# Kernel tuning notes

Measured on AMD Instinct MI355X. Metric: run time of the kernel, lower is better.

The kernel has to match this reference:

```python
import jax, jax.numpy as jnp
import numpy as np

DIM = 768
HEADS = 12
HIDDEN = 3072  # dim * mlp_ratio
EPS = 1e-5


def layernorm(x, g, b):
    mu = jnp.mean(x, axis=-1, keepdims=True)
    var = jnp.var(x, axis=-1, keepdims=True)
    return (x - mu) * jax.lax.rsqrt(var + EPS) * g + b


def setup_inputs() -> dict:
    key = jax.random.key(0)
    ks = jax.random.split(key, 10)
    s = 0.02
    return {
        "x": jax.random.normal(ks[0], (4, 1024, DIM), jnp.float32),
        "attention_mask": jax.random.randint(ks[1], (4, 1024), 0, 2, jnp.int32),
        "ln1_g": jnp.ones((DIM,), jnp.float32),
        "ln1_b": jnp.zeros((DIM,), jnp.float32),
        "ln2_g": jnp.ones((DIM,), jnp.float32),
        "ln2_b": jnp.zeros((DIM,), jnp.float32),
        "w_qkv": jax.random.normal(ks[2], (DIM, 3 * DIM), jnp.float32) * s,
        "b_qkv": jnp.zeros((3 * DIM,), jnp.float32),
        "w_proj": jax.random.normal(ks[3], (DIM, DIM), jnp.float32) * s,
        "b_proj": jnp.zeros((DIM,), jnp.float32),
        "w_fc1": jax.random.normal(ks[4], (DIM, HIDDEN), jnp.float32) * s,
        "b_fc1": jnp.zeros((HIDDEN,), jnp.float32),
        "w_fc2": jax.random.normal(ks[5], (HIDDEN, DIM), jnp.float32) * s,
        "b_fc2": jnp.zeros((DIM,), jnp.float32),
    }


def reference(x, attention_mask, ln1_g, ln1_b, ln2_g, ln2_b,
              w_qkv, b_qkv, w_proj, b_proj, w_fc1, b_fc1, w_fc2, b_fc2):
    B, N, C = x.shape
    hd = C // HEADS
    scale = hd ** -0.5

    # --- attention branch ---
    h = layernorm(x, ln1_g, ln1_b)
    qkv = (h @ w_qkv + b_qkv).reshape(B, N, 3, HEADS, hd)
    q, k, v = qkv[:, :, 0], qkv[:, :, 1], qkv[:, :, 2]  # [B,N,H,hd]
    attn = jnp.einsum('bnhd,bmhd->bhnm', q, k) * scale
    mask_bias = jnp.where(attention_mask == 0, -10000.0, 0.0)[:, None, None, :]
    attn = jax.nn.softmax(attn + mask_bias, axis=-1)
    o = jnp.einsum('bhnm,bmhd->bnhd', attn, v).reshape(B, N, C)
    x = x + (o @ w_proj + b_proj)

    # --- MLP branch ---
    h = layernorm(x, ln2_g, ln2_b)
    h = jax.nn.gelu(h @ w_fc1 + b_fc1, approximate=False)
    x = x + (h @ w_fc2 + b_fc2)
    return x
```

## Files before the change

### kernel.cpp

```cpp
#include <hip/hip_runtime.h>

#define DIM 768
#define NTOK 4096
#define HID 3072

typedef __attribute__((ext_vector_type(8))) short bf16x8;
typedef __attribute__((ext_vector_type(4))) float f32x4;

__device__ inline unsigned short f2bf(float f){
  unsigned u = __float_as_uint(f);
  u += 0x7fff + ((u >> 16) & 1);
  return (unsigned short)(u >> 16);
}
__device__ inline unsigned cvt_pk_bf16(float a, float b){
  unsigned r;
  asm("v_cvt_pk_bf16_f32 %0, %1, %2" : "=v"(r) : "v"(a), "v"(b));
  return r;
}
__device__ inline void gload_lds16(const void* g, void* l){
  __builtin_amdgcn_global_load_lds(
      (const __attribute__((address_space(1))) unsigned int*)g,
      (__attribute__((address_space(3))) unsigned int*)l, 16, 0, 0);
}
template<int N> __device__ inline void wait_vmcnt(){
  if constexpr (N == 0) asm volatile("s_waitcnt vmcnt(0)" ::: "memory");
  else if constexpr (N == 4) asm volatile("s_waitcnt vmcnt(4)" ::: "memory");
  else if constexpr (N == 8) asm volatile("s_waitcnt vmcnt(8)" ::: "memory");
  else static_assert(N == 0, "unsupported vmcnt");
}
__device__ inline int swz_read(int row, int hi){
  return (row * 64 + hi * 16) ^ ((row & 7) << 4);
}

__global__ __launch_bounds__(256) void ln_kernel(const float* __restrict__ x,
    const float* __restrict__ g, const float* __restrict__ b,
    unsigned short* __restrict__ out)
{
  int row = blockIdx.x * 4 + (threadIdx.x >> 6);
  int lane = threadIdx.x & 63;
  const float* xr = x + (size_t)row * DIM;
  float4 v[3];
  float s = 0.f, s2 = 0.f;
#pragma unroll
  for (int j = 0; j < 3; ++j){
    v[j] = *(const float4*)(xr + j * 256 + lane * 4);
    s  += v[j].x + v[j].y + v[j].z + v[j].w;
    s2 += v[j].x*v[j].x + v[j].y*v[j].y + v[j].z*v[j].z + v[j].w*v[j].w;
  }
#pragma unroll
  for (int m = 1; m < 64; m <<= 1){ s += __shfl_xor(s, m, 64); s2 += __shfl_xor(s2, m, 64); }
  float mu  = s * (1.f / 768.f);
  float var = s2 * (1.f / 768.f) - mu * mu;
  float inv = rsqrtf(var + 1e-5f);
#pragma unroll
  for (int j = 0; j < 3; ++j){
    int c0 = j * 256 + lane * 4;
    float vv[4] = { v[j].x, v[j].y, v[j].z, v[j].w };
    ushort4 o4;
    o4.x = f2bf((vv[0] - mu) * inv * g[c0 + 0] + b[c0 + 0]);
    o4.y = f2bf((vv[1] - mu) * inv * g[c0 + 1] + b[c0 + 1]);
    o4.z = f2bf((vv[2] - mu) * inv * g[c0 + 2] + b[c0 + 2]);
    o4.w = f2bf((vv[3] - mu) * inv * g[c0 + 3] + b[c0 + 3]);
    *(ushort4*)(out + (size_t)row * DIM + c0) = o4;
  }
}

__global__ __launch_bounds__(256) void transpose4_kernel(
    const float* __restrict__ w_qkv, const float* __restrict__ w_proj,
    const float* __restrict__ w_fc1, const float* __restrict__ w_fc2,
    unsigned short* __restrict__ tq, unsigned short* __restrict__ tp,
    unsigned short* __restrict__ t1, unsigned short* __restrict__ t2)
{
  __shared__ __align__(16) unsigned short tile[32][33];
  int id = blockIdx.x;
  const float* W; unsigned short* Wt; int K, N, tx_n;
  if (id < 1728)      { W = w_qkv;  Wt = tq; K = 768;  N = 2304; tx_n = 72; }
  else if (id < 2304) { W = w_proj; Wt = tp; K = 768;  N = 768;  tx_n = 24; id -= 1728; }
  else if (id < 4608) { W = w_fc1;  Wt = t1; K = 768;  N = 3072; tx_n = 96; id -= 2304; }
  else                { W = w_fc2;  Wt = t2; K = 3072; N = 768;  tx_n = 24; id -= 4608; }
  int n0 = (id % tx_n) * 32, k0 = (id / tx_n) * 32;
  int tx = threadIdx.x & 31, ty = threadIdx.x >> 5;
#pragma unroll
  for (int i = 0; i < 32; i += 8)
    tile[ty + i][tx] = f2bf(W[(size_t)(k0 + ty + i) * N + n0 + tx]);
  __syncthreads();
#pragma unroll
  for (int i = 0; i < 32; i += 8)
    Wt[(size_t)(n0 + ty + i) * K + k0 + tx] = tile[tx][ty + i];
}

__global__ __launch_bounds__(256) void pack_mask_kernel(const int* __restrict__ am,
    unsigned long long* __restrict__ pm)
{
  int lane = threadIdx.x & 63, w = threadIdx.x >> 6, b = blockIdx.x;
  for (int k = w; k < 16; k += 4){
    unsigned long long m = __ballot(am[b * 1024 + k * 64 + lane] != 0);
    if (lane == 0) pm[b * 16 + k] = m;
  }
}

__global__ __launch_bounds__(256) void gemm_qkv_kernel(
    const unsigned short* __restrict__ A,
    const unsigned short* __restrict__ Bt,
    const float* __restrict__ bias,
    unsigned short* __restrict__ q_out,
    unsigned short* __restrict__ k_out,
    unsigned short* __restrict__ v_out,
    int M, int N, int K)
{
  constexpr int BM = 128, BN = 96, BK = 32, DEPTH = 3;
  constexpr int MI = 4, NI = 3;
  constexpr int SMEM_B = DEPTH * (BM + BN) * BK * 2;
  __shared__ __align__(16) char smem[SMEM_B];
  auto As = (unsigned short(*)[BM * BK])smem;
  auto Bs = (unsigned short(*)[BN * BK])(smem + DEPTH * BM * BK * 2);
  const int t = threadIdx.x, lane = t & 63, wid = t >> 6;
  const int lo = lane & 15, hi = lane >> 4;
  const int wr = wid >> 1, wc = wid & 1;

  const int gx = gridDim.x;
  const int nwg = gx * gridDim.y;
  const int lin = blockIdx.y * gx + blockIdx.x;
  const int swz = (lin & 7) * (nwg >> 3) + (lin >> 3);
  const int bm = (swz / gx) * BM, bn = (swz % gx) * BN;

  const unsigned short *p0, *p1, *p2, *p3;
  int d3;
  {
    int c, rp, r, q;
    c = t;       rp = c >> 2; r = rp ^ ((rp >> 2) & 1); q = (c & 3) ^ (r & 3);
    p0 = A  + (size_t)(bm + r) * K + q * 8;
    c = 256 + t; rp = c >> 2; r = rp ^ ((rp >> 2) & 1); q = (c & 3) ^ (r & 3);
    p1 = A  + (size_t)(bm + r) * K + q * 8;
    c = t;       rp = c >> 2; r = rp ^ ((rp >> 2) & 1); q = (c & 3) ^ (r & 3);
    p2 = Bt + (size_t)(bn + r) * K + q * 8;
    int c2w = (t < 128) ? 256 + t : t - 128;
    c = c2w;     rp = c >> 2; r = rp ^ ((rp >> 2) & 1); q = (c & 3) ^ (r & 3);
    p3 = Bt + (size_t)(bn + r) * K + q * 8;
    d3 = c2w * 8;
  }
  int ofsA[MI], ofsB[NI];
#pragma unroll
  for (int i = 0; i < MI; ++i) ofsA[i] = swz_read(wr * 64 + i * 16 + lo, hi);
#pragma unroll
  for (int j = 0; j < NI; ++j) ofsB[j] = swz_read(wc * 48 + j * 16 + lo, hi);

  f32x4 acc[MI][NI];
#pragma unroll
  for (int i = 0; i < MI; ++i)
#pragma unroll
    for (int j = 0; j < NI; ++j) acc[i][j] = (f32x4){0.f, 0.f, 0.f, 0.f};

  const int NIT = K / BK;
  auto stagefull = [&](int buf) __attribute__((always_inline)) {
    gload_lds16(p0, &As[buf][t * 8]);
    gload_lds16(p1, &As[buf][(256 + t) * 8]);
    gload_lds16(p2, &Bs[buf][t * 8]);
    gload_lds16(p3, &Bs[buf][d3]);
    p0 += BK; p1 += BK; p2 += BK; p3 += BK;
  };
  auto kbody = [&](int it, int RB, int WB) __attribute__((always_inline)) {
    if (it < NIT - 1) wait_vmcnt<4>(); else wait_vmcnt<0>();
    __builtin_amdgcn_sched_barrier(0);
    __builtin_amdgcn_s_barrier();
    __builtin_amdgcn_sched_barrier(0);
    if (it + 2 < NIT) stagefull(WB);
    const char* as = (const char*)As[RB];
    const char* bs = (const char*)Bs[RB];
    bf16x8 af[MI], bfr[NI];
#pragma unroll
    for (int i = 0; i < MI; ++i) af[i]  = *(const bf16x8*)(as + ofsA[i]);
#pragma unroll
    for (int j = 0; j < NI; ++j) bfr[j] = *(const bf16x8*)(bs + ofsB[j]);
#pragma unroll
    for (int i = 0; i < MI; ++i)
#pragma unroll
      for (int j = 0; j < NI; ++j)
        acc[i][j] = __builtin_amdgcn_mfma_f32_16x16x32_bf16(af[i], bfr[j], acc[i][j], 0, 0, 0);
  };

  stagefull(0);
  stagefull(1);
  for (int it = 0; it < NIT; it += 3){
    kbody(it,     0, 2);
    kbody(it + 1, 1, 0);
    kbody(it + 2, 2, 1);
  }

  __syncthreads();

  const int part = bn / 768;
  const int cloc = bn % 768;
  const int bb = bm >> 10, n0b = bm & 1023;
  unsigned short* ET = (unsigned short*)smem;
  if (part < 2){
    constexpr int LDE = 104;
#pragma unroll
    for (int i = 0; i < MI; ++i)
#pragma unroll
      for (int j = 0; j < NI; ++j){
        int col_l = wc * 48 + j * 16 + lo;
        float bcol = bias[bn + col_l];
#pragma unroll
        for (int r = 0; r < 4; ++r)
          ET[(wr * 64 + i * 16 + hi * 4 + r) * LDE + col_l] = f2bf(acc[i][j][r] + bcol);
      }
    __syncthreads();
    unsigned short* dst0 = (part == 0) ? q_out : k_out;
#pragma unroll
    for (int p = 0; p < 8; ++p){
      int row = p * 16 + (t >> 4), chunk = t & 15;
      if (chunk < 12){
        int col = cloc + chunk * 8, hh = col >> 6, d0 = col & 63;
        *(bf16x8*)&dst0[((size_t)(bb * 12 + hh)) * 65536 + (n0b + row) * 64 + d0] =
            *(const bf16x8*)&ET[row * LDE + chunk * 8];
      }
    }
  } else {
    constexpr int LDV = 136;
#pragma unroll
    for (int i = 0; i < MI; ++i)
#pragma unroll
      for (int j = 0; j < NI; ++j){
        int col_l = wc * 48 + j * 16 + lo;
        float bcol = bias[bn + col_l];
#pragma unroll
        for (int r = 0; r < 4; ++r)
          ET[col_l * LDV + wr * 64 + i * 16 + hi * 4 + r] = f2bf(acc[i][j][r] + bcol);
      }
    __syncthreads();
#pragma unroll
    for (int p = 0; p < 6; ++p){
      int colg = p * 16 + (t >> 4), chunk = t & 15;
      int col = cloc + colg, hh = col >> 6, d = col & 63;
      *(bf16x8*)&v_out[((size_t)(bb * 12 + hh)) * 65536 + (size_t)d * 1024 + n0b + chunk * 8] =
          *(const bf16x8*)&ET[colg * LDV + chunk * 8];
    }
  }
}

template<int EPI>
__global__ __launch_bounds__(512) void gemm_ks_kernel(
    const unsigned short* __restrict__ A,
    const unsigned short* __restrict__ Bt,
    const float* __restrict__ bias,
    const float* __restrict__ resid,
    void* __restrict__ Cout,
    int M, int N, int K)
{
  constexpr int BM = 128, BN = 96, BK = 64, DEPTH = 3;
  constexpr int MI = 4, NI = 3;
  constexpr int ACH = BM * BK / 8;
  constexpr int BCH = BN * BK / 8;
  constexpr int NC = 4;
  constexpr int TILE_A = BM * BK * 2, TILE_B = BN * BK * 2;
  constexpr int LDE = BN + 4;
  constexpr int SMEM_B = (DEPTH * (TILE_A + TILE_B) > BM * LDE * 4)
                       ?  DEPTH * (TILE_A + TILE_B) : BM * LDE * 4;
  __shared__ __align__(16) char smem[SMEM_B];
  auto As = (unsigned short(*)[BM * BK])smem;
  auto Bs = (unsigned short(*)[BN * BK])(smem + DEPTH * TILE_A);
  const int t = threadIdx.x, lane = t & 63, wid = t >> 6;
  const int lo = lane & 15, hi = lane >> 4;
  const int ks = wid & 1, wc = (wid >> 1) & 1, wr = wid >> 2;

  const int gx = gridDim.x;
  const int nwg = gx * gridDim.y;
  const int lin = blockIdx.y * gx + blockIdx.x;
  const int swz = (lin & 7) * (nwg >> 3) + (lin >> 3);
  const int bm = (swz / gx) * BM, bn = (swz % gx) * BN;

  auto stage = [&](int buf, int k0){
#pragma unroll
    for (int u = 0; u < NC; ++u){
      int c = u * 512 + t;
      if (c < ACH){
        int r = c >> 3, q = (c & 7) ^ (r & 7);
        gload_lds16(A + (size_t)(bm + r) * K + k0 + q * 8, &As[buf][c * 8]);
      } else {
        int c2 = c - ACH;
        if (c2 >= BCH) c2 -= BCH;
        int r = c2 >> 3, q = (c2 & 7) ^ (r & 7);
        gload_lds16(Bt + (size_t)(bn + r) * K + k0 + q * 8, &Bs[buf][c2 * 8]);
      }
    }
  };
  auto rd = [&](const char* base, int row, int q)->bf16x8 {
    return *(const bf16x8*)(base + row * 128 + ((q ^ (row & 7)) << 4));
  };

  f32x4 acc[MI][NI];
#pragma unroll
  for (int i = 0; i < MI; ++i)
#pragma unroll
    for (int j = 0; j < NI; ++j) acc[i][j] = (f32x4){0.f, 0.f, 0.f, 0.f};

  const int NIT = K / BK;
  stage(0, 0);
  stage(1, BK);
  const int qk = ks * 4 + hi;
  for (int it = 0; it < NIT; ++it){
    if (it < NIT - 1) wait_vmcnt<NC>();
    else wait_vmcnt<0>();
    __builtin_amdgcn_sched_barrier(0);
    __builtin_amdgcn_s_barrier();
    __builtin_amdgcn_sched_barrier(0);
    if (it + 2 < NIT) stage((it + 2) % DEPTH, (it + 2) * BK);
    const char* as = (const char*)As[it % DEPTH];
    const char* bs = (const char*)Bs[it % DEPTH];
    bf16x8 af[MI], bfr[NI];
#pragma unroll
    for (int i = 0; i < MI; ++i)  af[i]  = rd(as, wr * 64 + i * 16 + lo, qk);
#pragma unroll
    for (int j = 0; j < NI; ++j) bfr[j] = rd(bs, wc * 48 + j * 16 + lo, qk);
#pragma unroll
    for (int i = 0; i < MI; ++i)
#pragma unroll
      for (int j = 0; j < NI; ++j)
        acc[i][j] = __builtin_amdgcn_mfma_f32_16x16x32_bf16(af[i], bfr[j], acc[i][j], 0, 0, 0);
  }

  __syncthreads();
  float* ET = (float*)smem;
  if (ks == 1){
#pragma unroll
    for (int i = 0; i < MI; ++i)
#pragma unroll
      for (int j = 0; j < NI; ++j)
#pragma unroll
        for (int r = 0; r < 4; ++r)
          ET[(wr * 64 + i * 16 + hi * 4 + r) * LDE + wc * 48 + j * 16 + lo] = acc[i][j][r];
  }
  __syncthreads();
  if (ks == 0){
#pragma unroll
    for (int i = 0; i < MI; ++i)
#pragma unroll
      for (int j = 0; j < NI; ++j){
        int col_l = wc * 48 + j * 16 + lo;
        float bcol = bias[bn + col_l];
#pragma unroll
        for (int r = 0; r < 4; ++r){
          int idx = (wr * 64 + i * 16 + hi * 4 + r) * LDE + col_l;
          ET[idx] = ET[idx] + acc[i][j][r] + bcol;
        }
      }
  }
  __syncthreads();
  if constexpr (EPI == 2){
    int row = t >> 2, q = t & 3;
    const float* rrow = resid + (size_t)(bm + row) * N + bn;
    float* crow = (float*)Cout + (size_t)(bm + row) * N + bn;
#pragma unroll
    for (int k = 0; k < 6; ++k){
      int c4 = (q + k * 4) * 4;
      float4 v = *(const float4*)&ET[row * LDE + c4];
      float4 rs = *(const float4*)&rrow[c4];
      v.x += rs.x; v.y += rs.y; v.z += rs.z; v.w += rs.w;
      *(float4*)&crow[c4] = v;
    }
  } else {
    int row = t >> 2, cq = t & 3;
    unsigned short* crow = (unsigned short*)Cout + (size_t)(bm + row) * N + bn;
#pragma unroll
    for (int s = 0; s < 3; ++s){
      int c0 = cq * 8 + s * 32;
      unsigned w4[4];
#pragma unroll
      for (int e = 0; e < 4; ++e){
        float x0 = ET[row * LDE + c0 + e * 2];
        float x1 = ET[row * LDE + c0 + e * 2 + 1];
        x0 = 0.5f * x0 * (1.f + erff(x0 * 0.70710678118f));
        x1 = 0.5f * x1 * (1.f + erff(x1 * 0.70710678118f));
        w4[e] = (unsigned)f2bf(x0) | ((unsigned)f2bf(x1) << 16);
      }
      *(uint4*)&crow[c0] = make_uint4(w4[0], w4[1], w4[2], w4[3]);
    }
  }
}

__global__ __launch_bounds__(256) void attn_kernel(
    const unsigned short* __restrict__ Qs,
    const unsigned short* __restrict__ Ks,
    const unsigned short* __restrict__ Vts,
    const unsigned long long* __restrict__ pm,
    unsigned short* __restrict__ o)
{
  constexpr int LD = 72;
  __shared__ __align__(16) unsigned short Kl[2][64 * LD];
  __shared__ __align__(16) unsigned short Vt[2][64 * LD];
  __shared__ __align__(16) unsigned short Pl[4][16 * LD];
  const int qb = blockIdx.x, h = blockIdx.y, b = blockIdx.z;
  const int t = threadIdx.x, wid = t >> 6, lane = t & 63;
  const int lo = lane & 15, hi = lane >> 4;
  const size_t bh = (size_t)b * 12 + h;

  const unsigned short* Qg = Qs + (bh * 1024 + qb * 64 + wid * 16 + lo) * 64;
  bf16x8 qf0 = *(const bf16x8*)(Qg + hi * 8);
  bf16x8 qf1 = *(const bf16x8*)(Qg + 32 + hi * 8);

  f32x4 oacc[4];
#pragma unroll
  for (int dj = 0; dj < 4; ++dj) oacc[dj] = (f32x4){0.f, 0.f, 0.f, 0.f};
  float l_part = 0.f;

  const int srow = t >> 2, scol = (t & 3) * 16;
  const int sdst = srow * LD + scol;
  const unsigned short* kg = Ks  + bh * 65536 + srow * 64 + scol;
  const unsigned short* vg = Vts + bh * 65536 + srow * 1024 + scol;
  unsigned short* pw = &Pl[wid][0];

  bf16x8 kn0 = *(const bf16x8*)(kg);
  bf16x8 kn1 = *(const bf16x8*)(kg + 8);
  bf16x8 vn0 = *(const bf16x8*)(vg);
  bf16x8 vn1 = *(const bf16x8*)(vg + 8);
  *(bf16x8*)&Kl[0][sdst]     = kn0;
  *(bf16x8*)&Kl[0][sdst + 8] = kn1;
  *(bf16x8*)&Vt[0][sdst]     = vn0;
  *(bf16x8*)&Vt[0][sdst + 8] = vn1;
  __syncthreads();

  for (int kt = 0; kt < 16; ++kt){
    const int cur = kt & 1;
    if (kt + 1 < 16){
      kn0 = *(const bf16x8*)(kg + (kt + 1) * 4096);
      kn1 = *(const bf16x8*)(kg + (kt + 1) * 4096 + 8);
      vn0 = *(const bf16x8*)(vg + (kt + 1) * 64);
      vn1 = *(const bf16x8*)(vg + (kt + 1) * 64 + 8);
    }

    f32x4 s[4];
#pragma unroll
    for (int nj = 0; nj < 4; ++nj) s[nj] = (f32x4){0.f, 0.f, 0.f, 0.f};
#pragma unroll
    for (int kk = 0; kk < 2; ++kk){
      bf16x8 q = kk ? qf1 : qf0;
#pragma unroll
      for (int nj = 0; nj < 4; ++nj){
        bf16x8 kf = *(const bf16x8*)&Kl[cur][(nj * 16 + lo) * LD + kk * 32 + hi * 8];
        s[nj] = __builtin_amdgcn_mfma_f32_16x16x32_bf16(kf, q, s[nj], 0, 0, 0);
      }
    }

    unsigned long long w = pm[b * 16 + kt] >> (hi * 4);
#pragma unroll
    for (int nj = 0; nj < 4; ++nj){
      float p[4];
#pragma unroll
      for (int r = 0; r < 4; ++r){
        float e = __expf(fmaf(s[nj][r], 0.125f, -16.0f));
        e = ((unsigned)(w >> (nj * 16 + r)) & 1u) ? e : 0.0f;
        l_part += e;
        p[r] = e;
      }
      unsigned w0 = cvt_pk_bf16(p[0], p[1]);
      unsigned w1 = cvt_pk_bf16(p[2], p[3]);
      *(uint2*)&pw[lo * LD + nj * 16 + hi * 4] = make_uint2(w0, w1);
    }
    asm volatile("" ::: "memory");
    bf16x8 pf0 = *(const bf16x8*)&pw[lo * LD + hi * 8];
    bf16x8 pf1 = *(const bf16x8*)&pw[lo * LD + 32 + hi * 8];
#pragma unroll
    for (int kk = 0; kk < 2; ++kk){
      bf16x8 pf = kk ? pf1 : pf0;
#pragma unroll
      for (int dj = 0; dj < 4; ++dj){
        bf16x8 vf = *(const bf16x8*)&Vt[cur][(dj * 16 + lo) * LD + kk * 32 + hi * 8];
        oacc[dj] = __builtin_amdgcn_mfma_f32_16x16x32_bf16(vf, pf, oacc[dj], 0, 0, 0);
      }
    }

    if (kt + 1 < 16){
      *(bf16x8*)&Kl[cur ^ 1][sdst]     = kn0;
      *(bf16x8*)&Kl[cur ^ 1][sdst + 8] = kn1;
      *(bf16x8*)&Vt[cur ^ 1][sdst]     = vn0;
      *(bf16x8*)&Vt[cur ^ 1][sdst + 8] = vn1;
    }
    __syncthreads();
  }

  float l = l_part;
  l += __shfl_xor(l, 16, 64);
  l += __shfl_xor(l, 32, 64);
  float inv = 1.0f / l;
  size_t orow = (size_t)b * 1024 + qb * 64 + wid * 16 + lo;
#pragma unroll
  for (int dj = 0; dj < 4; ++dj){
    unsigned w0 = (unsigned)f2bf(oacc[dj][0] * inv) | ((unsigned)f2bf(oacc[dj][1] * inv) << 16);
    unsigned w1 = (unsigned)f2bf(oacc[dj][2] * inv) | ((unsigned)f2bf(oacc[dj][3] * inv) << 16);
    *(uint2*)&o[orow * DIM + h * 64 + dj * 16 + hi * 4] = make_uint2(w0, w1);
  }
}

extern "C" void kernel_launch(void* const* d_in, const int* in_sizes, int n_in,
                              void* d_out, int out_size, void* d_ws, size_t ws_size,
                              hipStream_t stream)
{
  const float* x      = (const float*)d_in[0];
  const int*   amask  = (const int*)  d_in[1];
  const float* ln1_g  = (const float*)d_in[2];
  const float* ln1_b  = (const float*)d_in[3];
  const float* ln2_g  = (const float*)d_in[4];
  const float* ln2_b  = (const float*)d_in[5];
  const float* w_qkv  = (const float*)d_in[6];
  const float* b_qkv  = (const float*)d_in[7];
  const float* w_proj = (const float*)d_in[8];
  const float* b_proj = (const float*)d_in[9];
  const float* w_fc1  = (const float*)d_in[10];
  const float* b_fc1  = (const float*)d_in[11];
  const float* w_fc2  = (const float*)d_in[12];
  const float* b_fc2  = (const float*)d_in[13];
  float* outp = (float*)d_out;

  char* w = (char*)d_ws;
  auto alloc = [&](size_t bytes){ char* p = w; w += (bytes + 255) & ~(size_t)255; return p; };

  char* p0 = alloc((size_t)4 * 6291456);
  unsigned short* Qs   = (unsigned short*)p0;
  unsigned short* Ks   = (unsigned short*)(p0 + 6291456);
  unsigned short* Vts  = (unsigned short*)(p0 + 2 * 6291456);
  unsigned short* o_bf = (unsigned short*)(p0 + 3 * 6291456);
  unsigned short* a1   = (unsigned short*)p0;
  unsigned short* h_bf = (unsigned short*)alloc((size_t)NTOK * DIM * 2);
  unsigned short* h2   = h_bf;
  float*          x1   = (float*)alloc((size_t)NTOK * DIM * 4);
  unsigned short* wqkvT = (unsigned short*)alloc((size_t)3 * DIM * DIM * 2);
  unsigned short* wprojT= (unsigned short*)alloc((size_t)DIM * DIM * 2);
  unsigned short* wfc1T = (unsigned short*)alloc((size_t)HID * DIM * 2);
  unsigned short* wfc2T = (unsigned short*)alloc((size_t)DIM * HID * 2);
  unsigned long long* pmask = (unsigned long long*)alloc(4 * 16 * 8);

  transpose4_kernel<<<6912, 256, 0, stream>>>(w_qkv, w_proj, w_fc1, w_fc2,
                                              wqkvT, wprojT, wfc1T, wfc2T);
  pack_mask_kernel<<<4, 256, 0, stream>>>(amask, pmask);

  ln_kernel<<<NTOK / 4, 256, 0, stream>>>(x, ln1_g, ln1_b, h_bf);
  gemm_qkv_kernel<<<dim3(2304 / 96, NTOK / 128), 256, 0, stream>>>(
      h_bf, wqkvT, b_qkv, Qs, Ks, Vts, NTOK, 2304, DIM);
  attn_kernel<<<dim3(16, 12, 4), 256, 0, stream>>>(Qs, Ks, Vts, pmask, o_bf);
  gemm_ks_kernel<2><<<dim3(DIM / 96, NTOK / 128), 512, 0, stream>>>(
      o_bf, wprojT, b_proj, x, x1, NTOK, DIM, DIM);
  ln_kernel<<<NTOK / 4, 256, 0, stream>>>(x1, ln2_g, ln2_b, h2);
  gemm_ks_kernel<1><<<dim3(HID / 96, NTOK / 128), 512, 0, stream>>>(
      h2, wfc1T, b_fc1, nullptr, a1, NTOK, HID, DIM);
  gemm_ks_kernel<2><<<dim3(DIM / 96, NTOK / 128), 512, 0, stream>>>(
      a1, wfc2T, b_fc2, x1, outp, NTOK, DIM, HID);
}
```

Before: 171.1 us.

## Use dedicated 128x128 GEMM with fused GELU for FC1 and raise MFMA priority

```diff
diff --git a/kernel.cpp b/kernel.cpp
--- a/kernel.cpp
+++ b/kernel.cpp
@@ -172,11 +172,13 @@
     for (int i = 0; i < MI; ++i) af[i]  = *(const bf16x8*)(as + ofsA[i]);
 #pragma unroll
     for (int j = 0; j < NI; ++j) bfr[j] = *(const bf16x8*)(bs + ofsB[j]);
+    __builtin_amdgcn_s_setprio(1);
 #pragma unroll
     for (int i = 0; i < MI; ++i)
 #pragma unroll
       for (int j = 0; j < NI; ++j)
         acc[i][j] = __builtin_amdgcn_mfma_f32_16x16x32_bf16(af[i], bfr[j], acc[i][j], 0, 0, 0);
+    __builtin_amdgcn_s_setprio(0);
   };
 
   stagefull(0);
@@ -240,12 +242,120 @@
 }
 
 template<int EPI>
+__global__ __launch_bounds__(256) void gemm_kernel(
+    const unsigned short* __restrict__ A,
+    const unsigned short* __restrict__ Bt,
+    const float* __restrict__ bias,
+    unsigned short* __restrict__ C,
+    int M, int N, int K)
+{
+  constexpr int BM = 128, BN = 128, BK = 32, WM = 64, WN = 64, DEPTH = 3;
+  constexpr int MI = WM / 16, NI = WN / 16;
+  constexpr int SMEM_B = DEPTH * (BM + BN) * BK * 2;
+  __shared__ __align__(16) char smem[SMEM_B];
+  auto As = (unsigned short(*)[BM * BK])smem;
+  auto Bs = (unsigned short(*)[BN * BK])(smem + DEPTH * BM * BK * 2);
+  const int t = threadIdx.x, lane = t & 63, wid = t >> 6;
+  const int lo = lane & 15, hi = lane >> 4;
+  const int wr = wid >> 1, wc = wid & 1;
+
+  const int gx = gridDim.x;
+  const int nwg = gx * gridDim.y;
+  const int lin = blockIdx.y * gx + blockIdx.x;
+  const int swz = (lin & 7) * (nwg >> 3) + (lin >> 3);
+  const int bm = (swz / gx) * BM, bn = (swz % gx) * BN;
+
+  const unsigned short *a0, *a1, *b0, *b1;
+  {
+    int rp = t >> 2, r = rp ^ ((rp >> 2) & 1), q = (t & 3) ^ (r & 3);
+    a0 = A  + (size_t)(bm + r) * K + q * 8;
+    b0 = Bt + (size_t)(bn + r) * K + q * 8;
+    int c = 256 + t;
+    rp = c >> 2; r = rp ^ ((rp >> 2) & 1); q = (c & 3) ^ (r & 3);
+    a1 = A  + (size_t)(bm + r) * K + q * 8;
+    b1 = Bt + (size_t)(bn + r) * K + q * 8;
+  }
+  int ofsA[MI], ofsB[NI];
+#pragma unroll
+  for (int i = 0; i < MI; ++i) ofsA[i] = swz_read(wr * WM + i * 16 + lo, hi);
+#pragma unroll
+  for (int j = 0; j < NI; ++j) ofsB[j] = swz_read(wc * WN + j * 16 + lo, hi);
+
+  f32x4 acc[MI][NI];
+#pragma unroll
+  for (int i = 0; i < MI; ++i)
+#pragma unroll
+    for (int j = 0; j < NI; ++j) acc[i][j] = (f32x4){0.f, 0.f, 0.f, 0.f};
+
+  const int NIT = K / BK;
+  auto stagefull = [&](int buf) __attribute__((always_inline)) {
+    gload_lds16(a0, &As[buf][t * 8]);
+    gload_lds16(a1, &As[buf][(256 + t) * 8]);
+    gload_lds16(b0, &Bs[buf][t * 8]);
+    gload_lds16(b1, &Bs[buf][(256 + t) * 8]);
+    a0 += BK; a1 += BK; b0 += BK; b1 += BK;
+  };
+  auto kbody = [&](int it, int RB, int WB) __attribute__((always_inline)) {
+    if (it < NIT - 1) wait_vmcnt<4>(); else wait_vmcnt<0>();
+    __builtin_amdgcn_sched_barrier(0);
+    __builtin_amdgcn_s_barrier();
+    __builtin_amdgcn_sched_barrier(0);
+    if (it + 2 < NIT) stagefull(WB);
+    const char* as = (const char*)As[RB];
+    const char* bs = (const char*)Bs[RB];
+    bf16x8 af[MI], bfr[NI];
+#pragma unroll
+    for (int i = 0; i < MI; ++i) af[i]  = *(const bf16x8*)(as + ofsA[i]);
+#pragma unroll
+    for (int j = 0; j < NI; ++j) bfr[j] = *(const bf16x8*)(bs + ofsB[j]);
+    __builtin_amdgcn_s_setprio(1);
+#pragma unroll
+    for (int i = 0; i < MI; ++i)
+#pragma unroll
+      for (int j = 0; j < NI; ++j)
+        acc[i][j] = __builtin_amdgcn_mfma_f32_16x16x32_bf16(af[i], bfr[j], acc[i][j], 0, 0, 0);
+    __builtin_amdgcn_s_setprio(0);
+  };
+
+  stagefull(0);
+  stagefull(1);
+  for (int it = 0; it < NIT; it += 3){
+    kbody(it,     0, 2);
+    kbody(it + 1, 1, 0);
+    kbody(it + 2, 2, 1);
+  }
+
+  __syncthreads();
+
+  constexpr int LDE = BN + 8;
+  unsigned short* ET = (unsigned short*)smem;
+#pragma unroll
+  for (int i = 0; i < MI; ++i)
+#pragma unroll
+    for (int j = 0; j < NI; ++j){
+      float bcol = bias[bn + wc * WN + j * 16 + lo];
+#pragma unroll
+      for (int r = 0; r < 4; ++r){
+        float v = acc[i][j][r] + bcol;
+        if constexpr (EPI == 1) v = 0.5f * v * (1.f + erff(v * 0.70710678118f));
+        ET[(wr * WM + i * 16 + hi * 4 + r) * LDE + wc * WN + j * 16 + lo] = f2bf(v);
+      }
+    }
+  __syncthreads();
+#pragma unroll
+  for (int p = 0; p < BM / 16; ++p){
+    int row = p * 16 + (t >> 4), chunk = t & 15;
+    *(bf16x8*)&C[(size_t)(bm + row) * N + bn + chunk * 8] =
+        *(const bf16x8*)&ET[row * LDE + chunk * 8];
+  }
+}
+
 __global__ __launch_bounds__(512) void gemm_ks_kernel(
     const unsigned short* __restrict__ A,
     const unsigned short* __restrict__ Bt,
     const float* __restrict__ bias,
     const float* __restrict__ resid,
-    void* __restrict__ Cout,
+    float* __restrict__ C,
     int M, int N, int K)
 {
   constexpr int BM = 128, BN = 96, BK = 64, DEPTH = 3;
@@ -313,11 +423,13 @@
     for (int i = 0; i < MI; ++i)  af[i]  = rd(as, wr * 64 + i * 16 + lo, qk);
 #pragma unroll
     for (int j = 0; j < NI; ++j) bfr[j] = rd(bs, wc * 48 + j * 16 + lo, qk);
+    __builtin_amdgcn_s_setprio(1);
 #pragma unroll
     for (int i = 0; i < MI; ++i)
 #pragma unroll
       for (int j = 0; j < NI; ++j)
         acc[i][j] = __builtin_amdgcn_mfma_f32_16x16x32_bf16(af[i], bfr[j], acc[i][j], 0, 0, 0);
+    __builtin_amdgcn_s_setprio(0);
   }
 
   __syncthreads();
@@ -347,10 +459,10 @@
       }
   }
   __syncthreads();
-  if constexpr (EPI == 2){
+  {
     int row = t >> 2, q = t & 3;
     const float* rrow = resid + (size_t)(bm + row) * N + bn;
-    float* crow = (float*)Cout + (size_t)(bm + row) * N + bn;
+    float* crow = C + (size_t)(bm + row) * N + bn;
 #pragma unroll
     for (int k = 0; k < 6; ++k){
       int c4 = (q + k * 4) * 4;
@@ -358,23 +470,6 @@
       float4 rs = *(const float4*)&rrow[c4];
       v.x += rs.x; v.y += rs.y; v.z += rs.z; v.w += rs.w;
       *(float4*)&crow[c4] = v;
-    }
-  } else {
-    int row = t >> 2, cq = t & 3;
-    unsigned short* crow = (unsigned short*)Cout + (size_t)(bm + row) * N + bn;
-#pragma unroll
-    for (int s = 0; s < 3; ++s){
-      int c0 = cq * 8 + s * 32;
-      unsigned w4[4];
-#pragma unroll
-      for (int e = 0; e < 4; ++e){
-        float x0 = ET[row * LDE + c0 + e * 2];
-        float x1 = ET[row * LDE + c0 + e * 2 + 1];
-        x0 = 0.5f * x0 * (1.f + erff(x0 * 0.70710678118f));
-        x1 = 0.5f * x1 * (1.f + erff(x1 * 0.70710678118f));
-        w4[e] = (unsigned)f2bf(x0) | ((unsigned)f2bf(x1) << 16);
-      }
-      *(uint4*)&crow[c0] = make_uint4(w4[0], w4[1], w4[2], w4[3]);
     }
   }
 }
@@ -432,6 +527,7 @@
     f32x4 s[4];
 #pragma unroll
     for (int nj = 0; nj < 4; ++nj) s[nj] = (f32x4){0.f, 0.f, 0.f, 0.f};
+    __builtin_amdgcn_s_setprio(1);
 #pragma unroll
     for (int kk = 0; kk < 2; ++kk){
       bf16x8 q = kk ? qf1 : qf0;
@@ -441,6 +537,7 @@
         s[nj] = __builtin_amdgcn_mfma_f32_16x16x32_bf16(kf, q, s[nj], 0, 0, 0);
       }
     }
+    __builtin_amdgcn_s_setprio(0);
 
     unsigned long long w = pm[b * 16 + kt] >> (hi * 4);
 #pragma unroll
@@ -460,6 +557,7 @@
     asm volatile("" ::: "memory");
     bf16x8 pf0 = *(const bf16x8*)&pw[lo * LD + hi * 8];
     bf16x8 pf1 = *(const bf16x8*)&pw[lo * LD + 32 + hi * 8];
+    __builtin_amdgcn_s_setprio(1);
 #pragma unroll
     for (int kk = 0; kk < 2; ++kk){
       bf16x8 pf = kk ? pf1 : pf0;
@@ -469,6 +567,7 @@
         oacc[dj] = __builtin_amdgcn_mfma_f32_16x16x32_bf16(vf, pf, oacc[dj], 0, 0, 0);
       }
     }
+    __builtin_amdgcn_s_setprio(0);
 
     if (kt + 1 < 16){
       *(bf16x8*)&Kl[cur ^ 1][sdst]     = kn0;
@@ -538,11 +637,11 @@
   gemm_qkv_kernel<<<dim3(2304 / 96, NTOK / 128), 256, 0, stream>>>(
       h_bf, wqkvT, b_qkv, Qs, Ks, Vts, NTOK, 2304, DIM);
   attn_kernel<<<dim3(16, 12, 4), 256, 0, stream>>>(Qs, Ks, Vts, pmask, o_bf);
-  gemm_ks_kernel<2><<<dim3(DIM / 96, NTOK / 128), 512, 0, stream>>>(
+  gemm_ks_kernel<<<dim3(DIM / 96, NTOK / 128), 512, 0, stream>>>(
       o_bf, wprojT, b_proj, x, x1, NTOK, DIM, DIM);
   ln_kernel<<<NTOK / 4, 256, 0, stream>>>(x1, ln2_g, ln2_b, h2);
-  gemm_ks_kernel<1><<<dim3(HID / 96, NTOK / 128), 512, 0, stream>>>(
-      h2, wfc1T, b_fc1, nullptr, a1, NTOK, HID, DIM);
-  gemm_ks_kernel<2><<<dim3(DIM / 96, NTOK / 128), 512, 0, stream>>>(
+  gemm_kernel<1><<<dim3(HID / 128, NTOK / 128), 256, 0, stream>>>(
+      h2, wfc1T, b_fc1, a1, NTOK, HID, DIM);
+  gemm_ks_kernel<<<dim3(DIM / 96, NTOK / 128), 512, 0, stream>>>(
       a1, wfc2T, b_fc2, x1, outp, NTOK, DIM, HID);
 }
```

After: 157.1 us. 8.2% less time.
